# Kernel tuning notes

Measured on AMD Instinct MI355X. Metric: run time of the kernel, lower is better.

The kernel has to match this reference:

```python
import jax, jax.numpy as jnp
import numpy as np

B, S = 128, 512
VOCAB, E, H, T = 100000, 100, 128, 10  # tagset_size=10 -> CRF over T-1=9 tags
HD = H // 2  # per-direction LSTM hidden


def setup_inputs():
    key = jax.random.key(0)
    ks = jax.random.split(key, 14)
    s = 0.08
    inputs = jax.random.randint(ks[0], (B, S), 1, VOCAB)
    tags = jax.random.randint(ks[1], (B, S), 1, T)  # valid after tags-1 shift
    mask = jnp.ones((B, S), dtype=bool)
    emb = (jax.random.normal(ks[2], (VOCAB, E)) * s).at[0].set(0.0)  # padding_idx=0 row zeroed
    Wih_f = jax.random.normal(ks[3], (4 * HD, E)) * s
    Whh_f = jax.random.normal(ks[4], (4 * HD, HD)) * s
    b_f = jax.random.normal(ks[5], (4 * HD,)) * s
    Wih_b = jax.random.normal(ks[6], (4 * HD, E)) * s
    Whh_b = jax.random.normal(ks[7], (4 * HD, HD)) * s
    b_b = jax.random.normal(ks[8], (4 * HD,)) * s
    W_out = jax.random.normal(ks[9], (T, H)) * s
    b_out = jax.random.normal(ks[10], (T,)) * s
    start = jax.random.normal(ks[11], (T - 1,)) * s
    end = jax.random.normal(ks[12], (T - 1,)) * s
    trans = jax.random.normal(ks[13], (T - 1, T - 1)) * s
    return dict(inputs=inputs, tags=tags, mask=mask, emb=emb,
                Wih_f=Wih_f, Whh_f=Whh_f, b_f=b_f,
                Wih_b=Wih_b, Whh_b=Whh_b, b_b=b_b,
                W_out=W_out, b_out=b_out, start=start, end=end, trans=trans)


def _lstm_dir(x, Wih, Whh, b, reverse):
    # x: [S, B, E] time-major; PyTorch gate order i,f,g,o; b = b_ih + b_hh
    h0 = jnp.zeros((x.shape[1], Whh.shape[1]), x.dtype)

    def step(carry, xt):
        h, c = carry
        gates = xt @ Wih.T + h @ Whh.T + b
        i, f, g, o = jnp.split(gates, 4, axis=-1)
        c = jax.nn.sigmoid(f) * c + jax.nn.sigmoid(i) * jnp.tanh(g)
        h = jax.nn.sigmoid(o) * jnp.tanh(c)
        return (h, c), h

    _, hs = jax.lax.scan(step, (h0, h0), x, reverse=reverse)
    return hs  # [S, B, HD]


def _crf_nll(em, tags, mask, start, end, trans):
    # Linear-chain CRF (torchcrf-style). em: [S,B,K], tags/mask: [S,B]
    pick = lambda e, t: jnp.take_along_axis(e, t[:, None], axis=-1)[:, 0]
    # numerator: score of the gold path
    score0 = start[tags[0]] + pick(em[0], tags[0])

    def num_step(sc, inp):
        em_t, t, tp, m = inp
        return sc + jnp.where(m, trans[tp, t] + pick(em_t, t), 0.0), None

    score, _ = jax.lax.scan(num_step, score0, (em[1:], tags[1:], tags[:-1], mask[1:]))
    last_idx = mask.sum(0).astype(jnp.int32) - 1
    last_tags = jnp.take_along_axis(tags, last_idx[None, :], axis=0)[0]
    score = score + end[last_tags]
    # denominator: forward algorithm (log partition)
    alpha0 = start[None, :] + em[0]  # [B,K]

    def fwd_step(alpha, inp):
        em_t, m = inp
        nxt = jax.nn.logsumexp(alpha[:, :, None] + trans[None, :, :] + em_t[:, None, :], axis=1)
        return jnp.where(m[:, None], nxt, alpha), None

    alpha, _ = jax.lax.scan(fwd_step, alpha0, (em[1:], mask[1:]))
    logZ = jax.nn.logsumexp(alpha + end[None, :], axis=1)
    return -(score - logZ).mean()  # loss = -log_likelihood.mean()


def _forward(inputs, tags, mask, emb, Wih_f, Whh_f, b_f, Wih_b, Whh_b, b_b, W_out, b_out, start, end, trans):
    x = emb[inputs].transpose(1, 0, 2)  # [S,B,E]
    h = jnp.concatenate([_lstm_dir(x, Wih_f, Whh_f, b_f, False),
                         _lstm_dir(x, Wih_b, Whh_b, b_b, True)], axis=-1)  # [S,B,H]
    # dropout is identity at eval; slice off tag 0 as in the module
    em = (h @ W_out.T + b_out)[:, :, 1:]  # [S,B,T-1]
    return _crf_nll(em, (tags - 1).T, mask.T, start, end, trans)


def reference(inputs, tags, mask, emb, Wih_f, Whh_f, b_f, Wih_b, Whh_b, b_b, W_out, b_out, start, end, trans):
    return _forward(inputs, tags, mask, emb, Wih_f, Whh_f, b_f, Wih_b, Whh_b, b_b, W_out, b_out, start, end, trans)
```

## Files before the change

kernel.cpp:

```cpp
#include <hip/hip_runtime.h>
#include <math.h>

#define SB 512
#define NB 128
#define HD 64

typedef _Float16 h2 __attribute__((ext_vector_type(2)));
union U4 { uint4 u; h2 h[4]; _Float16 f[8]; };
union U2 { uint2 u; _Float16 f[4]; };
union UH { unsigned u; _Float16 f[2]; };

__device__ __forceinline__ float frcp(float x) { return __builtin_amdgcn_rcpf(x); }
__device__ __forceinline__ float fsig(float x) { return frcp(1.0f + __expf(-x)); }
__device__ __forceinline__ float ftanh(float x) {
    float t = __expf(-2.0f * fabsf(x));
    float r = (1.0f - t) * frcp(1.0f + t);
    return copysignf(r, x);
}
__device__ __forceinline__ float fdot2(h2 a, h2 b, float c) {
    return __builtin_amdgcn_fdot2(a, b, c, false);
}

__global__ void prep_kernel(const float* __restrict__ Wih_f, const float* __restrict__ Wih_bb,
                            const float* __restrict__ Whh_f, const float* __restrict__ Whh_bb,
                            const float* __restrict__ b_f, const float* __restrict__ b_bb,
                            const float* __restrict__ trans,
                            unsigned* __restrict__ W2h, unsigned* __restrict__ whh16,
                            float* __restrict__ bias2, float* __restrict__ Eexp)
{
    int idx = blockIdx.x * 256 + threadIdx.x;
    if (idx < 26624) {
        int col = idx / 52, d = idx - col * 52;
        int dir = col >> 8, r = col & 255, j = r >> 2, g = r & 3;
        const float* src = (dir ? Wih_bb : Wih_f) + (g * 64 + j) * 100;
        UH u; u.u = 0;
        if (d < 50) { u.f[0] = (_Float16)src[2 * d]; u.f[1] = (_Float16)src[2 * d + 1]; }
        W2h[idx] = u.u;
    } else if (idx < 43008) {
        int d = idx - 26624;
        int kp = d & 31, u = (d >> 5) & 63, g = (d >> 11) & 3, dir = d >> 13;
        const float* src = (dir ? Whh_bb : Whh_f) + (g * 64 + u) * 64 + 2 * kp;
        UH uu; uu.f[0] = (_Float16)src[0]; uu.f[1] = (_Float16)src[1];
        int k4 = kp >> 2, q = kp & 3;
        whh16[(((dir * 4 + g) * 8 + k4) * 64 + u) * 4 + q] = uu.u;
    } else if (idx < 43520) {
        int col = idx - 43008;
        int dir = col >> 8, r = col & 255, j = r >> 2, g = r & 3;
        bias2[col] = (dir ? b_bb : b_f)[g * 64 + j];
    } else if (idx < 43601) {
        int i = idx - 43520;
        Eexp[i] = __expf(trans[i]);
    }
}

__global__ __launch_bounds__(256, 1) void gemm_kernel(
    const int* __restrict__ inputs, const float* __restrict__ emb,
    const unsigned* __restrict__ W2h, const float* __restrict__ bias2,
    _Float16* __restrict__ xgh)
{
    __shared__ __align__(16) unsigned sE[128 * 52];
    __shared__ __align__(16) unsigned sW[128 * 52];
    __shared__ int stok[128];
    const int tt = blockIdx.x;
    const int tid = threadIdx.x;

    if (tid < 128) stok[tid] = inputs[tid * SB + tt];
    __syncthreads();
    for (int idx = tid; idx < 6656; idx += 256) {
        int row = idx / 52, d = idx - row * 52;
        int token = stok[row];
        UH u; u.u = 0;
        if (d < 50) {
            const float* ep = emb + (size_t)token * 100 + 2 * d;
            u.f[0] = (_Float16)ep[0]; u.f[1] = (_Float16)ep[1];
        }
        sE[idx] = u.u;
    }

    const int tx = tid & 15, ty = tid >> 4;

    for (int cb4 = 0; cb4 < 4; ++cb4) {
        const int cb = cb4 * 128;
        __syncthreads();
        for (int idx = tid; idx < 1664; idx += 256)
            ((uint4*)sW)[idx] = ((const uint4*)W2h)[cb * 13 + idx];
        __syncthreads();

        float acc[8][8];
        #pragma unroll
        for (int r = 0; r < 8; ++r)
            #pragma unroll
            for (int i = 0; i < 8; ++i) acc[r][i] = 0.f;

        for (int kk = 0; kk < 13; ++kk) {
            U4 e[8], wv[8];
            #pragma unroll
            for (int r = 0; r < 8; ++r) e[r].u = ((const uint4*)sE)[(ty + 16 * r) * 13 + kk];
            #pragma unroll
            for (int i = 0; i < 8; ++i) wv[i].u = ((const uint4*)sW)[(tx + 16 * i) * 13 + kk];
            #pragma unroll
            for (int r = 0; r < 8; ++r)
                #pragma unroll
                for (int i = 0; i < 8; ++i) {
                    float a = acc[r][i];
                    #pragma unroll
                    for (int q = 0; q < 4; ++q) a = fdot2(e[r].h[q], wv[i].h[q], a);
                    acc[r][i] = a;
                }
        }

        #pragma unroll
        for (int i = 0; i < 8; ++i) {
            int col = cb + tx + 16 * i;
            float bc = bias2[col];
            #pragma unroll
            for (int r = 0; r < 8; ++r) {
                int row = tt * NB + ty + 16 * r;
                xgh[(size_t)row * 512 + col] = (_Float16)(acc[r][i] + bc);
            }
        }
    }
}

__global__ __attribute__((amdgpu_flat_work_group_size(64, 64), amdgpu_waves_per_eu(1, 1)))
void lstm_kernel(
    const _Float16* __restrict__ xgh, const unsigned* __restrict__ whh16,
    _Float16* __restrict__ h16)
{
    const int blk = blockIdx.x;
    const int b = blk & (NB - 1);
    const int dir = blk >> 7;
    const int j = threadIdx.x;

    __shared__ __align__(16) unsigned wlds[8192];
    __shared__ __align__(16) _Float16 hbuf[64];

    {
        const uint4* src = (const uint4*)(whh16 + dir * 8192);
        uint4* dst = (uint4*)wlds;
        #pragma unroll
        for (int i = 0; i < 32; ++i) dst[i * 64 + j] = src[i * 64 + j];
    }
    hbuf[j] = (_Float16)0.f;
    float c = 0.f;

    const int t0 = dir ? (SB - 1) : 0;
    const ptrdiff_t xstride = (dir ? -1 : 1) * (ptrdiff_t)(NB * 512);
    const _Float16* xp = xgh + ((size_t)(t0 * NB + b)) * 512 + dir * 256 + j * 4;
    _Float16* hp = h16 + ((size_t)(b * 2 + dir) * SB + t0) * 64 + j;
    const ptrdiff_t hstride = (dir ? -1 : 1) * (ptrdiff_t)64;

    U2 p0, p1, p2;
    p0.u = *(const uint2*)xp;
    p1.u = *(const uint2*)(xp + xstride);
    p2.u = *(const uint2*)(xp + 2 * xstride);
    const _Float16* xq = xp + 3 * xstride;

    const uint4* wl = (const uint4*)wlds;

    for (int s = 0; s < SB; ++s) {
        float a0 = (float)p0.f[0], a1 = (float)p0.f[1];
        float a2 = (float)p0.f[2], a3 = (float)p0.f[3];
        p0 = p1; p1 = p2;
        p2.u = *(const uint2*)xq;
        xq += xstride;

        U4 hv[8];
        #pragma unroll
        for (int k4 = 0; k4 < 8; ++k4) hv[k4].u = *(const uint4*)&hbuf[k4 * 8];

        float g0[4] = {a0, 0.f, 0.f, 0.f};
        float g1[4] = {a1, 0.f, 0.f, 0.f};
        float g2[4] = {a2, 0.f, 0.f, 0.f};
        float g3[4] = {a3, 0.f, 0.f, 0.f};
        #pragma unroll
        for (int k4 = 0; k4 < 8; ++k4) {
            U4 w0, w1, w2, w3;
            w0.u = wl[(0 * 8 + k4) * 64 + j];
            w1.u = wl[(1 * 8 + k4) * 64 + j];
            w2.u = wl[(2 * 8 + k4) * 64 + j];
            w3.u = wl[(3 * 8 + k4) * 64 + j];
            const int p = k4 & 3;
            #pragma unroll
            for (int q = 0; q < 4; ++q) {
                g0[p] = fdot2(hv[k4].h[q], w0.h[q], g0[p]);
                g1[p] = fdot2(hv[k4].h[q], w1.h[q], g1[p]);
                g2[p] = fdot2(hv[k4].h[q], w2.h[q], g2[p]);
                g3[p] = fdot2(hv[k4].h[q], w3.h[q], g3[p]);
            }
        }
        a0 = (g0[0] + g0[1]) + (g0[2] + g0[3]);
        a1 = (g1[0] + g1[1]) + (g1[2] + g1[3]);
        a2 = (g2[0] + g2[1]) + (g2[2] + g2[3]);
        a3 = (g3[0] + g3[1]) + (g3[2] + g3[3]);

        float ig = fsig(a0), fg = fsig(a1), gg = ftanh(a2), og = fsig(a3);
        c = fg * c + ig * gg;
        float h = og * ftanh(c);
        *hp = (_Float16)h;
        hp += hstride;
        hbuf[j] = (_Float16)h;
    }
}

__global__ __launch_bounds__(256, 1) void proj_kernel(
    const _Float16* __restrict__ h16, const float* __restrict__ W_out,
    const float* __restrict__ b_out, float* __restrict__ em3)
{
    __shared__ __align__(16) unsigned tile[128 * 64];
    __shared__ __align__(16) unsigned sWo[9 * 64];
    __shared__ float sb[9];
    const int b = blockIdx.x, tid = threadIdx.x;

    for (int i2 = tid; i2 < 576; i2 += 256) {
        int k = i2 >> 6, jp = i2 & 63;
        const float* src = W_out + (k + 1) * 128 + 2 * jp;
        UH u; u.f[0] = (_Float16)src[0]; u.f[1] = (_Float16)src[1];
        sWo[i2] = u.u;
    }
    if (tid < 9) sb[tid] = b_out[1 + tid];

    float* dst0 = em3 + (size_t)b * (SB * 12);

    for (int tt = 0; tt < 4; ++tt) {
        const int t0 = tt * 128;
        __syncthreads();
        #pragma unroll
        for (int dir = 0; dir < 2; ++dir) {
            const unsigned* src = (const unsigned*)(h16 + ((size_t)(b * 2 + dir) * SB + t0) * 64);
            for (int i = tid; i < 4096; i += 256) {
                int t = i >> 5, jp = i & 31;
                tile[t * 64 + dir * 32 + jp] = src[i];
            }
        }
        __syncthreads();

        for (int o = tid; o < 1152; o += 256) {
            int tl = o / 9, k = o - 9 * tl;
            const U4* hr = (const U4*)&tile[tl * 64];
            const U4* wr = (const U4*)&sWo[k * 64];
            float pa = 0.f, pb = 0.f;
            #pragma unroll
            for (int q = 0; q < 16; q += 2) {
                U4 hv = hr[q], wv = wr[q];
                U4 hv2 = hr[q + 1], wv2 = wr[q + 1];
                #pragma unroll
                for (int z = 0; z < 4; ++z) {
                    pa = fdot2(hv.h[z], wv.h[z], pa);
                    pb = fdot2(hv2.h[z], wv2.h[z], pb);
                }
            }
            dst0[(t0 + tl) * 12 + k] = pa + pb + sb[k];
        }
    }
}

__global__ __launch_bounds__(64, 1) void crf_gold(
    const float* __restrict__ em3, const int* __restrict__ tags,
    const float* __restrict__ startv, const float* __restrict__ endv,
    const float* __restrict__ trans, float* __restrict__ gold)
{
    const int b = blockIdx.x, l = threadIdx.x;
    const int* tb = tags + (size_t)b * SB;
    const float* eb = em3 + (size_t)b * (SB * 12);
    float sc = 0.f;
    for (int t = l; t < SB; t += 64) {
        int tg = tb[t] - 1;
        if (t > 0) {
            int tp = tb[t - 1] - 1;
            sc += trans[tp * 9 + tg] + eb[t * 12 + tg];
        }
    }
    if (l == 0) {
        int tg0 = tb[0] - 1, tgl = tb[SB - 1] - 1;
        sc += startv[tg0] + eb[tg0] + endv[tgl];
    }
    #pragma unroll
    for (int off = 32; off > 0; off >>= 1) sc += __shfl_down(sc, off);
    if (l == 0) gold[b] = sc;
}

__global__ __launch_bounds__(256, 1) void crf_scan(
    const float* __restrict__ em3, const float* __restrict__ Eexp,
    float* __restrict__ Pws)
{
    const int lane = blockIdx.x * 256 + threadIdx.x;
    const int c = lane & 31, b = lane >> 5;

    float E[81];
    #pragma unroll
    for (int i = 0; i < 81; ++i) E[i] = Eexp[i];

    float P[81];
    #pragma unroll
    for (int i = 0; i < 81; ++i) P[i] = 0.f;
    #pragma unroll
    for (int i = 0; i < 9; ++i) P[i * 9 + i] = 1.f;
    float M = 0.f;

    const int t0 = 1 + 16 * c;
    const int nst = (t0 + 16 <= SB) ? 16 : (SB - t0);
    const float* ep = em3 + (size_t)b * (SB * 12) + t0 * 12;

    for (int s = 0; s < nst; ++s, ep += 12) {
        float4 e0 = *(const float4*)ep;
        float4 e1 = *(const float4*)(ep + 4);
        float e8 = ep[8];
        float ex[9] = { __expf(e0.x), __expf(e0.y), __expf(e0.z), __expf(e0.w),
                        __expf(e1.x), __expf(e1.y), __expf(e1.z), __expf(e1.w),
                        __expf(e8) };
        #pragma unroll
        for (int i = 0; i < 9; ++i) {
            float tmp[9];
            #pragma unroll
            for (int jj = 0; jj < 9; ++jj) tmp[jj] = P[i * 9] * E[jj];
            #pragma unroll
            for (int k = 1; k < 9; ++k)
                #pragma unroll
                for (int jj = 0; jj < 9; ++jj) tmp[jj] += P[i * 9 + k] * E[k * 9 + jj];
            #pragma unroll
            for (int jj = 0; jj < 9; ++jj) P[i * 9 + jj] = tmp[jj] * ex[jj];
        }
        if ((s & 3) == 3) {
            float mx = P[0];
            #pragma unroll
            for (int i = 1; i < 81; ++i) mx = fmaxf(mx, P[i]);
            M += __logf(mx);
            float r = frcp(mx);
            #pragma unroll
            for (int i = 0; i < 81; ++i) P[i] *= r;
        }
    }

    float* dst = Pws + (size_t)lane * 84;
    #pragma unroll
    for (int i = 0; i < 81; ++i) dst[i] = P[i];
    dst[81] = M;
}

__global__ __launch_bounds__(128, 1) void crf_combine(
    const float* __restrict__ em3, const float* __restrict__ Pws,
    const float* __restrict__ gold, const float* __restrict__ startv,
    const float* __restrict__ endv, float* __restrict__ out)
{
    const int b = threadIdx.x;
    float A[9], M = 0.f;
    {
        const float* eb = em3 + (size_t)b * (SB * 12);
        float4 e0 = *(const float4*)eb;
        float4 e1 = *(const float4*)(eb + 4);
        float e[9] = { e0.x, e0.y, e0.z, e0.w, e1.x, e1.y, e1.z, e1.w, eb[8] };
        #pragma unroll
        for (int k = 0; k < 9; ++k) A[k] = __expf(startv[k] + e[k]);
    }

    for (int c = 0; c < 32; ++c) {
        const float4* src = (const float4*)(Pws + ((size_t)b * 32 + c) * 84);
        float buf[84];
        #pragma unroll
        for (int q = 0; q < 21; ++q) {
            float4 v = src[q];
            buf[4 * q] = v.x; buf[4 * q + 1] = v.y; buf[4 * q + 2] = v.z; buf[4 * q + 3] = v.w;
        }
        float tmp[9];
        #pragma unroll
        for (int jj = 0; jj < 9; ++jj) tmp[jj] = A[0] * buf[jj];
        #pragma unroll
        for (int i = 1; i < 9; ++i)
            #pragma unroll
            for (int jj = 0; jj < 9; ++jj) tmp[jj] += A[i] * buf[i * 9 + jj];
        float mx = tmp[0];
        #pragma unroll
        for (int jj = 1; jj < 9; ++jj) mx = fmaxf(mx, tmp[jj]);
        M += __logf(mx) + buf[81];
        float r = frcp(mx);
        #pragma unroll
        for (int jj = 0; jj < 9; ++jj) A[jj] = tmp[jj] * r;
    }

    float Z = 0.f;
    #pragma unroll
    for (int k = 0; k < 9; ++k) Z += A[k] * __expf(endv[k]);
    float part = M + __logf(Z) - gold[b];

    #pragma unroll
    for (int off = 32; off > 0; off >>= 1) part += __shfl_down(part, off);
    __shared__ float sm[2];
    if ((b & 63) == 0) sm[b >> 6] = part;
    __syncthreads();
    if (b == 0) out[0] = (sm[0] + sm[1]) * (1.0f / NB);
}

extern "C" void kernel_launch(void* const* d_in, const int* in_sizes, int n_in,
                              void* d_out, int out_size, void* d_ws, size_t ws_size,
                              hipStream_t stream)
{
    const int*   inputs = (const int*)d_in[0];
    const int*   tags   = (const int*)d_in[1];
    const float* emb    = (const float*)d_in[3];
    const float* Wih_f  = (const float*)d_in[4];
    const float* Whh_f  = (const float*)d_in[5];
    const float* b_f    = (const float*)d_in[6];
    const float* Wih_b  = (const float*)d_in[7];
    const float* Whh_b  = (const float*)d_in[8];
    const float* b_b    = (const float*)d_in[9];
    const float* W_out  = (const float*)d_in[10];
    const float* b_out  = (const float*)d_in[11];
    const float* startv = (const float*)d_in[12];
    const float* endv   = (const float*)d_in[13];
    const float* transv = (const float*)d_in[14];

    char* w = (char*)d_ws;
    float* em3     = (float*)w;     w += (size_t)NB * SB * 12 * 4;
    _Float16* xgh  = (_Float16*)w;  w += (size_t)SB * NB * 512 * 2;
    _Float16* h16  = (_Float16*)w;  w += (size_t)NB * 2 * SB * 64 * 2;
    float* Pws     = (float*)w;     w += (size_t)NB * 32 * 84 * 4;
    float* gold    = (float*)w;     w += NB * 4;
    unsigned* W2h  = (unsigned*)w;  w += 26624 * 4;
    unsigned* whh16= (unsigned*)w;  w += 16384 * 4;
    float* bias2   = (float*)w;     w += 512 * 4;
    float* Eexp    = (float*)w;     w += 81 * 4;

    prep_kernel<<<171, 256, 0, stream>>>(Wih_f, Wih_b, Whh_f, Whh_b, b_f, b_b, transv,
                                         W2h, whh16, bias2, Eexp);
    gemm_kernel<<<SB, 256, 0, stream>>>(inputs, emb, W2h, bias2, xgh);
    lstm_kernel<<<256, 64, 0, stream>>>(xgh, whh16, h16);
    proj_kernel<<<NB, 256, 0, stream>>>(h16, W_out, b_out, em3);
    crf_gold<<<NB, 64, 0, stream>>>(em3, tags, startv, endv, transv, gold);
    crf_scan<<<16, 256, 0, stream>>>(em3, Eexp, Pws);
    crf_combine<<<1, 128, 0, stream>>>(em3, Pws, gold, startv, endv, (float*)d_out);
}
```

Measured before the change: 528.5 us.

## Use MFMA 16x16x32 f16 for input-projection GEMM with padded K layout

Replaces the fdot2-based register-tiled input projection GEMM with MFMA f16 matrix instructions, padding K from 100 to 128 halves (64 dwords per row) so it splits into four 32-wide MFMA steps. The prep kernel and workspace are resized to the padded weight layout, bias is staged in shared memory, and launch bounds now allow two blocks per CU. This targets the ALU cost of the embedding-times-Wih GEMM, at the price of extra padded zero work and more shared memory per block. The LSTM recurrence, which likely dominates total time, is unchanged.

```diff
diff --git a/kernel.cpp b/kernel.cpp
--- a/kernel.cpp
+++ b/kernel.cpp
@@ -6,7 +6,10 @@
 #define HD 64
 
 typedef _Float16 h2 __attribute__((ext_vector_type(2)));
+typedef _Float16 f16x8 __attribute__((ext_vector_type(8)));
+typedef float f32x4 __attribute__((ext_vector_type(4)));
 union U4 { uint4 u; h2 h[4]; _Float16 f[8]; };
+union UF { uint4 u; f16x8 h8; _Float16 f[8]; };
 union U2 { uint2 u; _Float16 f[4]; };
 union UH { unsigned u; _Float16 f[2]; };
 
@@ -29,96 +32,113 @@
                             float* __restrict__ bias2, float* __restrict__ Eexp)
 {
     int idx = blockIdx.x * 256 + threadIdx.x;
-    if (idx < 26624) {
-        int col = idx / 52, d = idx - col * 52;
+    if (idx < 32768) {
+        int col = idx >> 6, d = idx & 63;
         int dir = col >> 8, r = col & 255, j = r >> 2, g = r & 3;
         const float* src = (dir ? Wih_bb : Wih_f) + (g * 64 + j) * 100;
         UH u; u.u = 0;
         if (d < 50) { u.f[0] = (_Float16)src[2 * d]; u.f[1] = (_Float16)src[2 * d + 1]; }
         W2h[idx] = u.u;
-    } else if (idx < 43008) {
-        int d = idx - 26624;
+    } else if (idx < 49152) {
+        int d = idx - 32768;
         int kp = d & 31, u = (d >> 5) & 63, g = (d >> 11) & 3, dir = d >> 13;
         const float* src = (dir ? Whh_bb : Whh_f) + (g * 64 + u) * 64 + 2 * kp;
         UH uu; uu.f[0] = (_Float16)src[0]; uu.f[1] = (_Float16)src[1];
         int k4 = kp >> 2, q = kp & 3;
         whh16[(((dir * 4 + g) * 8 + k4) * 64 + u) * 4 + q] = uu.u;
-    } else if (idx < 43520) {
-        int col = idx - 43008;
+    } else if (idx < 49664) {
+        int col = idx - 49152;
         int dir = col >> 8, r = col & 255, j = r >> 2, g = r & 3;
         bias2[col] = (dir ? b_bb : b_f)[g * 64 + j];
-    } else if (idx < 43601) {
-        int i = idx - 43520;
+    } else if (idx < 49745) {
+        int i = idx - 49664;
         Eexp[i] = __expf(trans[i]);
     }
 }
 
-__global__ __launch_bounds__(256, 1) void gemm_kernel(
+__global__ __launch_bounds__(256, 2) void gemm_kernel(
     const int* __restrict__ inputs, const float* __restrict__ emb,
     const unsigned* __restrict__ W2h, const float* __restrict__ bias2,
     _Float16* __restrict__ xgh)
 {
-    __shared__ __align__(16) unsigned sE[128 * 52];
-    __shared__ __align__(16) unsigned sW[128 * 52];
+    __shared__ __align__(16) unsigned sE[128 * 64];
+    __shared__ __align__(16) unsigned sW[128 * 64];
+    __shared__ float sbias[512];
     __shared__ int stok[128];
     const int tt = blockIdx.x;
     const int tid = threadIdx.x;
+    const int w = tid >> 6, l = tid & 63;
+    const int q = l >> 4, n = l & 15;
 
     if (tid < 128) stok[tid] = inputs[tid * SB + tt];
+    for (int i = tid; i < 512; i += 256) sbias[i] = bias2[i];
     __syncthreads();
-    for (int idx = tid; idx < 6656; idx += 256) {
-        int row = idx / 52, d = idx - row * 52;
-        int token = stok[row];
-        UH u; u.u = 0;
+    for (int idx = tid; idx < 8192; idx += 256) {
+        int row = idx >> 6, d = idx & 63;
+        unsigned v = 0;
         if (d < 50) {
-            const float* ep = emb + (size_t)token * 100 + 2 * d;
-            u.f[0] = (_Float16)ep[0]; u.f[1] = (_Float16)ep[1];
-        }
-        sE[idx] = u.u;
-    }
-
-    const int tx = tid & 15, ty = tid >> 4;
-
-    for (int cb4 = 0; cb4 < 4; ++cb4) {
-        const int cb = cb4 * 128;
+            const float* ep = emb + (size_t)stok[row] * 100 + 2 * d;
+            UH u; u.f[0] = (_Float16)ep[0]; u.f[1] = (_Float16)ep[1];
+            v = u.u;
+        }
+        sE[idx] = v;
+    }
+
+    for (int cg = 0; cg < 4; ++cg) {
         __syncthreads();
-        for (int idx = tid; idx < 1664; idx += 256)
-            ((uint4*)sW)[idx] = ((const uint4*)W2h)[cb * 13 + idx];
+        for (int idx = tid; idx < 2048; idx += 256)
+            ((uint4*)sW)[idx] = ((const uint4*)W2h)[cg * 2048 + idx];
         __syncthreads();
 
-        float acc[8][8];
-        #pragma unroll
-        for (int r = 0; r < 8; ++r)
-            #pragma unroll
-            for (int i = 0; i < 8; ++i) acc[r][i] = 0.f;
-
-        for (int kk = 0; kk < 13; ++kk) {
-            U4 e[8], wv[8];
-            #pragma unroll
-            for (int r = 0; r < 8; ++r) e[r].u = ((const uint4*)sE)[(ty + 16 * r) * 13 + kk];
-            #pragma unroll
-            for (int i = 0; i < 8; ++i) wv[i].u = ((const uint4*)sW)[(tx + 16 * i) * 13 + kk];
-            #pragma unroll
-            for (int r = 0; r < 8; ++r)
+        f32x4 acc[2][8];
+        #pragma unroll
+        for (int m = 0; m < 2; ++m)
+            #pragma unroll
+            for (int c = 0; c < 8; ++c)
                 #pragma unroll
-                for (int i = 0; i < 8; ++i) {
-                    float a = acc[r][i];
-                    #pragma unroll
-                    for (int q = 0; q < 4; ++q) a = fdot2(e[r].h[q], wv[i].h[q], a);
-                    acc[r][i] = a;
+                for (int r = 0; r < 4; ++r) acc[m][c][r] = 0.f;
+
+        #pragma unroll
+        for (int kt = 0; kt < 4; ++kt) {
+            const int ko = 16 * kt + 2 * q;
+            UF A0, A1;
+            {
+                const unsigned* rp = &sE[(16 * (2 * w + 0) + n) * 64 + ko];
+                uint2 lo = *(const uint2*)rp;
+                uint2 hi = *(const uint2*)(rp + 8);
+                A0.u = make_uint4(lo.x, lo.y, hi.x, hi.y);
+                rp = &sE[(16 * (2 * w + 1) + n) * 64 + ko];
+                lo = *(const uint2*)rp;
+                hi = *(const uint2*)(rp + 8);
+                A1.u = make_uint4(lo.x, lo.y, hi.x, hi.y);
+            }
+            UF B[8];
+            #pragma unroll
+            for (int c = 0; c < 8; ++c) {
+                const unsigned* rp = &sW[(16 * c + n) * 64 + ko];
+                uint2 lo = *(const uint2*)rp;
+                uint2 hi = *(const uint2*)(rp + 8);
+                B[c].u = make_uint4(lo.x, lo.y, hi.x, hi.y);
+            }
+            #pragma unroll
+            for (int c = 0; c < 8; ++c) {
+                acc[0][c] = __builtin_amdgcn_mfma_f32_16x16x32_f16(A0.h8, B[c].h8, acc[0][c], 0, 0, 0);
+                acc[1][c] = __builtin_amdgcn_mfma_f32_16x16x32_f16(A1.h8, B[c].h8, acc[1][c], 0, 0, 0);
+            }
+        }
+
+        #pragma unroll
+        for (int m = 0; m < 2; ++m)
+            #pragma unroll
+            for (int c = 0; c < 8; ++c) {
+                int col = cg * 128 + 16 * c + n;
+                float bc = sbias[col];
+                #pragma unroll
+                for (int r = 0; r < 4; ++r) {
+                    int row = 16 * (2 * w + m) + 4 * q + r;
+                    xgh[(size_t)(tt * NB + row) * 512 + col] = (_Float16)(acc[m][c][r] + bc);
                 }
-        }
-
-        #pragma unroll
-        for (int i = 0; i < 8; ++i) {
-            int col = cb + tx + 16 * i;
-            float bc = bias2[col];
-            #pragma unroll
-            for (int r = 0; r < 8; ++r) {
-                int row = tt * NB + ty + 16 * r;
-                xgh[(size_t)row * 512 + col] = (_Float16)(acc[r][i] + bc);
-            }
-        }
+            }
     }
 }
 
@@ -241,9 +261,9 @@
             const U4* wr = (const U4*)&sWo[k * 64];
             float pa = 0.f, pb = 0.f;
             #pragma unroll
-            for (int q = 0; q < 16; q += 2) {
-                U4 hv = hr[q], wv = wr[q];
-                U4 hv2 = hr[q + 1], wv2 = wr[q + 1];
+            for (int qq = 0; qq < 16; qq += 2) {
+                U4 hv = hr[qq], wv = wr[qq];
+                U4 hv2 = hr[qq + 1], wv2 = wr[qq + 1];
                 #pragma unroll
                 for (int z = 0; z < 4; ++z) {
                     pa = fdot2(hv.h[z], wv.h[z], pa);
@@ -358,9 +378,9 @@
         const float4* src = (const float4*)(Pws + ((size_t)b * 32 + c) * 84);
         float buf[84];
         #pragma unroll
-        for (int q = 0; q < 21; ++q) {
-            float4 v = src[q];
-            buf[4 * q] = v.x; buf[4 * q + 1] = v.y; buf[4 * q + 2] = v.z; buf[4 * q + 3] = v.w;
+        for (int qq = 0; qq < 21; ++qq) {
+            float4 v = src[qq];
+            buf[4 * qq] = v.x; buf[4 * qq + 1] = v.y; buf[4 * qq + 2] = v.z; buf[4 * qq + 3] = v.w;
         }
         float tmp[9];
         #pragma unroll
@@ -416,12 +436,12 @@
     _Float16* h16  = (_Float16*)w;  w += (size_t)NB * 2 * SB * 64 * 2;
     float* Pws     = (float*)w;     w += (size_t)NB * 32 * 84 * 4;
     float* gold    = (float*)w;     w += NB * 4;
-    unsigned* W2h  = (unsigned*)w;  w += 26624 * 4;
+    unsigned* W2h  = (unsigned*)w;  w += 32768 * 4;
     unsigned* whh16= (unsigned*)w;  w += 16384 * 4;
     float* bias2   = (float*)w;     w += 512 * 4;
     float* Eexp    = (float*)w;     w += 81 * 4;
 
-    prep_kernel<<<171, 256, 0, stream>>>(Wih_f, Wih_b, Whh_f, Whh_b, b_f, b_b, transv,
+    prep_kernel<<<195, 256, 0, stream>>>(Wih_f, Wih_b, Whh_f, Whh_b, b_f, b_b, transv,
                                          W2h, whh16, bias2, Eexp);
     gemm_kernel<<<SB, 256, 0, stream>>>(inputs, emb, W2h, bias2, xgh);
     lstm_kernel<<<256, 64, 0, stream>>>(xgh, whh16, h16);
```

Result: slower. 547.4 us (+3.6%).
